# Kernel optimization log

Measured on AMD Instinct MI355X. Metric: run time of the kernel, lower is better.

Reference implementation:

```python
import jax, jax.numpy as jnp
import numpy as np

N_NODES = 50000
N_EDGES = 800000
IN, N1, N2, N3, N4, N5, L, NC = 7, 128, 128, 64, 64, 16, 16, 3


def _gat_params(key, fin, fout, edge_dim=1):
    ks = jax.random.split(key, 6)
    s = 0.1
    return dict(
        W=jax.random.normal(ks[0], (fin, fout), jnp.float32) * s,
        a_src=jax.random.normal(ks[1], (fout,), jnp.float32) * s,
        a_dst=jax.random.normal(ks[2], (fout,), jnp.float32) * s,
        We=jax.random.normal(ks[3], (edge_dim, fout), jnp.float32) * s,
        a_e=jax.random.normal(ks[4], (fout,), jnp.float32) * s,
        b=jax.random.normal(ks[5], (fout,), jnp.float32) * s,
    )


def setup_inputs() -> dict:
    key = jax.random.key(0)
    ks = jax.random.split(key, 16)
    inp = {
        'x1': jax.random.normal(ks[0], (N_NODES, IN), jnp.float32),
        'x2': jax.random.normal(ks[1], (N_NODES, IN), jnp.float32),
        'edge_index1': jax.random.randint(ks[2], (2, N_EDGES), 0, N_NODES),
        'edge_index2': jax.random.randint(ks[3], (2, N_EDGES), 0, N_NODES),
        'x_norm2_1': jax.random.normal(ks[4], (L,), jnp.float32),
        'x_norm2_2': jax.random.normal(ks[5], (L,), jnp.float32),
        'edge_col1': jax.random.uniform(ks[6], (N_EDGES, 1), jnp.float32),
        'edge_col2': jax.random.uniform(ks[7], (N_EDGES, 1), jnp.float32),
    }
    p1 = _gat_params(ks[8], IN, N1)
    p2 = _gat_params(ks[9], N1, N2)
    p3 = _gat_params(ks[10], N2, N3)
    for i, p in enumerate((p1, p2, p3), 1):
        for k, v in p.items():
            inp[f'{k}{i}'] = v
    s = 0.1
    inp['W_lin'] = jax.random.normal(ks[11], (N3 + L, N4), jnp.float32) * s
    inp['b_lin'] = jnp.zeros((N4,), jnp.float32)
    inp['W_c1'] = jax.random.normal(ks[12], (2 * N4, N5), jnp.float32) * s
    inp['b_c1'] = jnp.zeros((N5,), jnp.float32)
    inp['W_c2'] = jax.random.normal(ks[13], (N5, NC), jnp.float32) * s
    inp['b_c2'] = jnp.zeros((NC,), jnp.float32)
    return inp


def _gat_conv(x, src, dst, eattr, W, a_src, a_dst, We, a_e, b, n):
    # PyG GATConv, heads=1, add_self_loops with fill_value='mean'
    h = x @ W                                           # [N, C]
    ones = jnp.ones_like(dst, dtype=eattr.dtype)
    deg = jax.ops.segment_sum(ones, dst, n)
    loop_attr = jax.ops.segment_sum(eattr, dst, n) / jnp.maximum(deg, 1.0)[:, None]
    ar = jnp.arange(n, dtype=src.dtype)
    s = jnp.concatenate([src, ar])
    d = jnp.concatenate([dst, ar])
    ea = jnp.concatenate([eattr, loop_attr], axis=0)    # [E+N, edge_dim]
    alpha = (h @ a_src)[s] + (h @ a_dst)[d] + (ea @ We) @ a_e
    alpha = jax.nn.leaky_relu(alpha, 0.2)
    amax = jax.ops.segment_max(alpha, d, n)             # every node has a self loop
    ex = jnp.exp(alpha - amax[d])
    denom = jax.ops.segment_sum(ex, d, n)
    w = ex / denom[d]                                   # segment softmax weights
    out = jax.ops.segment_sum(w[:, None] * h[s], d, n)  # [N, C]
    return out + b


def _process_graph(x, ei, eattr, params):
    src, dst = ei[0], ei[1]
    n = x.shape[0]
    for p in params:
        x = jax.nn.elu(_gat_conv(x, src, dst, eattr, *p, n))
    return x.mean(axis=0)


def reference(x1, x2, edge_index1, edge_index2, x_norm2_1, x_norm2_2,
              edge_col1, edge_col2,
              W1, a_src1, a_dst1, We1, a_e1, b1,
              W2, a_src2, a_dst2, We2, a_e2, b2,
              W3, a_src3, a_dst3, We3, a_e3, b3,
              W_lin, b_lin, W_c1, b_c1, W_c2, b_c2):
    params = [
        (W1, a_src1, a_dst1, We1, a_e1, b1),
        (W2, a_src2, a_dst2, We2, a_e2, b2),
        (W3, a_src3, a_dst3, We3, a_e3, b3),
    ]
    g1 = _process_graph(x1, edge_index1, edge_col1, params)
    g2 = _process_graph(x2, edge_index2, edge_col2, params)
    g1 = jnp.concatenate([g1, x_norm2_1]) @ W_lin + b_lin
    g2 = jnp.concatenate([g2, x_norm2_2]) @ W_lin + b_lin
    x = jnp.concatenate([g1, g2])                       # [2*N4]
    h = jax.nn.relu(x @ W_c1 + b_c1)
    logits = h @ W_c2 + b_c2
    return logits[None, :]                              # [1, num_classes]
```

## Files before the change

kernel.cpp:

```cpp
#include <hip/hip_runtime.h>
#include <math.h>

#define NN 50000
#define NE 800000
#define NT 100000
#define NTP 100032
#define ET (2*NE + NT)
#define NPB 128
#define NBK 782
#define BCH 2048
#define BCAP 2816

typedef __attribute__((ext_vector_type(8))) short bf16x8;
typedef __attribute__((ext_vector_type(4))) float f32x4;

static __device__ __forceinline__ float wave_max64(float v){
  #pragma unroll
  for(int off=32;off;off>>=1) v = fmaxf(v, __shfl_xor(v,off));
  return v;
}
static __device__ __forceinline__ float wave_sum64(float v){
  #pragma unroll
  for(int off=32;off;off>>=1) v += __shfl_xor(v,off);
  return v;
}
static __device__ __forceinline__ unsigned short f2bf(float f){
  unsigned u = __float_as_uint(f);
  return (unsigned short)((u + 0x7FFFu + ((u>>16)&1u)) >> 16);
}
static __device__ __forceinline__ float bflo(unsigned v){ return __uint_as_float(v<<16); }
static __device__ __forceinline__ float bfhi(unsigned v){ return __uint_as_float(v & 0xFFFF0000u); }

__global__ __launch_bounds__(256) void k_hist(const int* __restrict__ d1,
    const int* __restrict__ d2, int* __restrict__ bcnt){
  __shared__ int h[1024];
  int t = threadIdx.x;
  #pragma unroll
  for (int i=0;i<4;i++) h[t + i*256] = 0;
  __syncthreads();
  int stride = gridDim.x*256;
  for (int e = blockIdx.x*256 + t; e < NE; e += stride){
    atomicAdd(&h[d1[e]>>7], 1);
    atomicAdd(&h[(d2[e]+NN)>>7], 1);
  }
  __syncthreads();
  #pragma unroll
  for (int i=0;i<4;i++){
    int idx = t + i*256;
    if (h[idx]) atomicAdd(&bcnt[idx], h[idx]);
  }
}

__global__ void k_hscan(const int* __restrict__ bcnt, int* __restrict__ hbase,
                        int* __restrict__ row_ptr){
  int t = threadIdx.x;
  int i0 = t*4;
  int c0=bcnt[i0], c1=bcnt[i0+1], c2=bcnt[i0+2], c3=bcnt[i0+3];
  int ts = c0+c1+c2+c3;
  int lane = t & 63, wv = t >> 6;
  int inc = ts;
  #pragma unroll
  for (int off=1; off<64; off<<=1){ int u = __shfl_up(inc, off); if (lane>=off) inc += u; }
  __shared__ int wsum[4];
  if (lane==63) wsum[wv] = inc;
  __syncthreads();
  int woff = 0;
  #pragma unroll
  for (int w=0; w<4; ++w) if (w < wv) woff += wsum[w];
  int run = woff + inc - ts;
  hbase[i0] = run; hbase[i0+1] = run+c0; hbase[i0+2] = run+c0+c1; hbase[i0+3] = run+c0+c1+c2;
  if (t==0) row_ptr[NT] = ET;
}

__global__ __launch_bounds__(256) void k_bin(const int* __restrict__ s1,
    const int* __restrict__ d1, const float* __restrict__ e1,
    const int* __restrict__ s2, const int* __restrict__ d2,
    const float* __restrict__ e2, const int* __restrict__ hbase,
    int* __restrict__ gcur, uint2* __restrict__ gstage){
  __shared__ int cnt[1024], loff[1024], cur[1024], gbase_sh[1024];
  __shared__ uint2 sdata[BCH];
  __shared__ unsigned short sbkt[BCH];
  __shared__ int wsum[4];
  int tid = threadIdx.x;
  int e0 = blockIdx.x*BCH;
  unsigned pack[8], eab[8];
  unsigned short bk[8];
  #pragma unroll
  for (int i=0;i<4;i++){ cnt[tid + i*256] = 0; cur[tid + i*256] = 0; }
  __syncthreads();
  #pragma unroll
  for (int u=0; u<8; ++u){
    int e = e0 + u*256 + tid;
    int b = NBK; unsigned p = 0, ea = 0;
    if (e < 2*NE){
      int src, dst; float eav;
      if (e < NE){ src = s1[e]; dst = d1[e]; eav = e1[e]; }
      else { int e2i = e - NE; src = s2[e2i] + NN; dst = d2[e2i] + NN; eav = e2[e2i]; }
      b = dst >> 7;
      p = (unsigned)src | ((unsigned)(dst & 127) << 17);
      ea = __float_as_uint(eav);
    }
    bk[u] = (unsigned short)b; pack[u] = p; eab[u] = ea;
    atomicAdd(&cnt[b], 1);
  }
  __syncthreads();
  {
    int i0 = tid*4;
    int c0=cnt[i0], c1=cnt[i0+1], c2=cnt[i0+2], c3=cnt[i0+3];
    int ts = c0+c1+c2+c3;
    int lane = tid & 63, wv = tid >> 6;
    int inc = ts;
    #pragma unroll
    for (int off=1; off<64; off<<=1){ int u = __shfl_up(inc, off); if (lane>=off) inc += u; }
    if (lane==63) wsum[wv] = inc;
    __syncthreads();
    int woff = 0;
    #pragma unroll
    for (int w=0; w<4; ++w) if (w < wv) woff += wsum[w];
    int run = woff + inc - ts;
    loff[i0] = run; loff[i0+1] = run+c0; loff[i0+2] = run+c0+c1; loff[i0+3] = run+c0+c1+c2;
  }
  for (int i = tid; i < NBK; i += 256)
    if (cnt[i] > 0) gbase_sh[i] = hbase[i] + atomicAdd(&gcur[i], cnt[i]);
  __syncthreads();
  #pragma unroll
  for (int u=0; u<8; ++u){
    int b = bk[u];
    int p = loff[b] + atomicAdd(&cur[b], 1);
    sdata[p] = make_uint2(pack[u], eab[u]);
    sbkt[p] = (unsigned short)b;
  }
  __syncthreads();
  for (int k = tid; k < BCH; k += 256){
    int b = sbkt[k];
    if (b < NBK) gstage[gbase_sh[b] + (k - loff[b])] = sdata[k];
  }
}

__global__ __launch_bounds__(256) void k_bucket(const uint2* __restrict__ gstage,
    const int* __restrict__ hbase, int2* __restrict__ srt, int* __restrict__ row_ptr){
  __shared__ uint2 sd[BCAP];
  __shared__ int deg[NPB], rbase[NPB], cur[NPB];
  __shared__ float easum[NPB];
  __shared__ int wsum[4];
  int b = blockIdx.x, t = threadIdx.x;
  int lo = b*NPB;
  int nloc = min(NPB, NT - lo);
  int est = hbase[b], ecnt = hbase[b+1] - est;
  bool inlds = (ecnt <= BCAP);
  if (t < NPB){ deg[t] = 0; easum[t] = 0.f; }
  __syncthreads();
  for (int k = t; k < ecnt; k += 256){
    uint2 v = gstage[est + k];
    if (inlds) sd[k] = v;
    int dl = v.x >> 17;
    atomicAdd(&deg[dl], 1);
    atomicAdd(&easum[dl], __uint_as_float(v.y));
  }
  __syncthreads();
  int dv = (t < nloc) ? deg[t] + 1 : 0;
  int lane = t & 63, wv = t >> 6;
  int inc = dv;
  #pragma unroll
  for (int off=1; off<64; off<<=1){ int u = __shfl_up(inc, off); if (lane>=off) inc += u; }
  if (lane==63) wsum[wv] = inc;
  __syncthreads();
  int woff = 0;
  #pragma unroll
  for (int w=0; w<4; ++w) if (w < wv) woff += wsum[w];
  int gb = est + lo + (woff + inc - dv);
  if (t < nloc){
    row_ptr[lo + t] = gb;
    rbase[t] = gb;
    cur[t] = 1;
    float se = easum[t] / fmaxf((float)deg[t], 1.f);
    srt[gb] = make_int2(lo + t, __float_as_int(se));
  }
  __syncthreads();
  for (int k = t; k < ecnt; k += 256){
    uint2 v = inlds ? sd[k] : gstage[est + k];
    int dl = v.x >> 17;
    int pos = rbase[dl] + atomicAdd(&cur[dl], 1);
    srt[pos] = make_int2((int)(v.x & 0x1FFFFu), (int)v.y);
  }
}

__global__ __launch_bounds__(256) void k_prep(
    const float* __restrict__ We0, const float* __restrict__ ae0,
    const float* __restrict__ We1, const float* __restrict__ ae1,
    const float* __restrict__ We2, const float* __restrict__ ae2,
    float* __restrict__ ce3, int* __restrict__ zbase,
    const float* __restrict__ W1, const float* __restrict__ W2,
    unsigned short* __restrict__ Wt1, unsigned short* __restrict__ Wt2){
  int t = threadIdx.x;
  for (int i = t; i < 1024+1024+128; i += 256) zbase[i] = 0;
  if (t < 64){
    const float* We[3] = {We0, We1, We2};
    const float* ae[3] = {ae0, ae1, ae2};
    const int fo[3] = {128, 128, 64};
    for (int L = 0; L < 3; ++L){
      float s = 0.f;
      for (int c = t; c < fo[L]; c += 64) s += We[L][c]*ae[L][c];
      s = wave_sum64(s);
      if (t == 0) ce3[L] = s;
    }
  }
  for (int i = t; i < 128*128; i += 256){
    int c = i >> 7, k = i & 127;
    Wt1[c*136 + k] = f2bf(W1[k*128 + c]);
  }
  for (int i = t; i < 64*128; i += 256){
    int c = i >> 7, k = i & 127;
    Wt2[c*136 + k] = f2bf(W2[k*64 + c]);
  }
}

template<int N>
__global__ __launch_bounds__(256) void k_gemm_mfma(
    const unsigned short* __restrict__ x16, const unsigned short* __restrict__ Wt,
    const float* __restrict__ a_src, const float* __restrict__ a_dst,
    unsigned short* __restrict__ h16, float* __restrict__ hs,
    float* __restrict__ hd, int n){
  constexpr int CT = N/16;
  __shared__ unsigned short Wl[N*136];
  int tid = threadIdx.x;
  for (int i = tid; i < N*136/8; i += 256)
    ((uint4*)Wl)[i] = ((const uint4*)Wt)[i];
  __syncthreads();
  int lane = tid & 63, w = tid >> 6;
  int arow = blockIdx.x*64 + w*16 + (lane & 15);
  int kb   = (lane >> 4) * 8;
  int rsafe = (arow < n) ? arow : (n-1);
  f32x4 acc[CT] = {};
  #pragma unroll
  for (int s = 0; s < 4; ++s){
    bf16x8 a = *(const bf16x8*)(x16 + (size_t)rsafe*128 + s*32 + kb);
    #pragma unroll
    for (int c = 0; c < CT; ++c){
      bf16x8 b = *(const bf16x8*)(&Wl[(c*16 + (lane&15))*136 + s*32 + kb]);
      acc[c] = __builtin_amdgcn_mfma_f32_16x16x32_bf16(a, b, acc[c], 0, 0, 0);
    }
  }
  int drow = blockIdx.x*64 + w*16 + (lane>>4)*4;
  int dcol = lane & 15;
  float psv[4] = {0,0,0,0}, pdv[4] = {0,0,0,0};
  #pragma unroll
  for (int c = 0; c < CT; ++c){
    float as = a_src[c*16 + dcol], ad = a_dst[c*16 + dcol];
    #pragma unroll
    for (int j = 0; j < 4; ++j){
      float v = acc[c][j];
      if (drow + j < n) h16[(size_t)(drow+j)*N + c*16 + dcol] = f2bf(v);
      psv[j] += v*as; pdv[j] += v*ad;
    }
  }
  #pragma unroll
  for (int off = 1; off < 16; off <<= 1){
    #pragma unroll
    for (int j=0;j<4;j++){ psv[j] += __shfl_xor(psv[j], off); pdv[j] += __shfl_xor(pdv[j], off); }
  }
  if (dcol == 0){
    #pragma unroll
    for (int j=0;j<4;j++) if (drow+j < n){ hs[drow+j] = psv[j]; hd[drow+j] = pdv[j]; }
  }
}

__global__ __launch_bounds__(256) void k_gemm7(const float* __restrict__ x1,
    const float* __restrict__ x2, const float* __restrict__ W,
    const float* __restrict__ a_src, const float* __restrict__ a_dst,
    unsigned short* __restrict__ h16, float* __restrict__ hs,
    float* __restrict__ hd, int n){
  __shared__ float Wl[7][128];
  int tid = threadIdx.x;
  for (int i = tid; i < 7*128; i += 256) ((float*)Wl)[i] = W[i];
  __syncthreads();
  int tx = tid & 31, ty = tid >> 5;
  int r = blockIdx.x*8 + ty;
  if (r >= n) return;
  const float* xr = (r < NN) ? (x1 + (size_t)r*7) : (x2 + (size_t)(r-NN)*7);
  float xv[7];
  #pragma unroll
  for (int k=0;k<7;k++) xv[k] = xr[k];
  float4 s = make_float4(0.f,0.f,0.f,0.f);
  #pragma unroll
  for (int k=0;k<7;k++){
    float4 wv = *(const float4*)(&Wl[k][tx*4]);
    s.x += xv[k]*wv.x; s.y += xv[k]*wv.y; s.z += xv[k]*wv.z; s.w += xv[k]*wv.w;
  }
  unsigned r0p = (unsigned)f2bf(s.x) | ((unsigned)f2bf(s.y)<<16);
  unsigned r1p = (unsigned)f2bf(s.z) | ((unsigned)f2bf(s.w)<<16);
  *(uint2*)(h16 + (size_t)r*128 + tx*4) = make_uint2(r0p, r1p);
  float ps = s.x*a_src[tx*4] + s.y*a_src[tx*4+1] + s.z*a_src[tx*4+2] + s.w*a_src[tx*4+3];
  float pd = s.x*a_dst[tx*4] + s.y*a_dst[tx*4+1] + s.z*a_dst[tx*4+2] + s.w*a_dst[tx*4+3];
  #pragma unroll
  for (int off=16; off; off>>=1){ ps += __shfl_xor(ps, off); pd += __shfl_xor(pd, off); }
  if (tx==0){ hs[r] = ps; hd[r] = pd; }
}

template<int FOUT, bool OBF>
__global__ __launch_bounds__(256) void k_aggregate(const unsigned short* __restrict__ h16,
    const float* __restrict__ hs, const float* __restrict__ hd,
    const int2* __restrict__ srt, const int* __restrict__ row_ptr,
    const float* __restrict__ ce_p, const float* __restrict__ b,
    void* __restrict__ xout, int n){
  constexpr int LPE = FOUT/8;
  constexpr int EPS = 64/LPE;
  __shared__ float s_p[4][64];
  __shared__ int   s_s[4][64];
  int tid = threadIdx.x;
  int wv = tid >> 6, lane = tid & 63;
  int wid = (int)((blockIdx.x*256 + tid) >> 6);
  if (wid >= n) return;
  float ce  = *ce_p;
  int beg = row_ptr[wid], end = row_ptr[wid+1];
  float hdn = hd[wid];
  int e_sub = lane / LPE;
  int col8  = (lane % LPE) * 8;
  float m = -INFINITY, den = 0.f;
  float acc[8] = {0.f,0.f,0.f,0.f,0.f,0.f,0.f,0.f};
  for (int base = beg; base < end; base += 64){
    int slot = base + lane;
    float a = -INFINITY; int src = 0;
    if (slot < end){
      int2 pk = srt[slot];
      src = pk.x;
      a = hs[src] + hdn + __int_as_float(pk.y)*ce;
      a = (a > 0.f) ? a : 0.2f*a;
    }
    float cm = wave_max64(a);
    float mnew = fmaxf(m, cm);
    float scale = __expf(m - mnew);
    den *= scale;
    #pragma unroll
    for (int u=0;u<8;u++) acc[u] *= scale;
    float p = __expf(a - mnew);
    den += wave_sum64(p);
    s_p[wv][lane] = p; s_s[wv][lane] = src;
    asm volatile("s_waitcnt lgkmcnt(0)" ::: "memory");
    int cnt = end - base; if (cnt > 64) cnt = 64;
    for (int j = 0; j < cnt; j += 2*EPS){
      int jj0 = j + e_sub, jj1 = j + EPS + e_sub;
      float p0 = s_p[wv][jj0];  int sj0 = s_s[wv][jj0];
      float p1 = s_p[wv][jj1];  int sj1 = s_s[wv][jj1];
      uint4 h0 = *(const uint4*)(h16 + (size_t)sj0*FOUT + col8);
      uint4 h1 = *(const uint4*)(h16 + (size_t)sj1*FOUT + col8);
      acc[0] += p0*bflo(h0.x); acc[1] += p0*bfhi(h0.x);
      acc[2] += p0*bflo(h0.y); acc[3] += p0*bfhi(h0.y);
      acc[4] += p0*bflo(h0.z); acc[5] += p0*bfhi(h0.z);
      acc[6] += p0*bflo(h0.w); acc[7] += p0*bfhi(h0.w);
      acc[0] += p1*bflo(h1.x); acc[1] += p1*bfhi(h1.x);
      acc[2] += p1*bflo(h1.y); acc[3] += p1*bfhi(h1.y);
      acc[4] += p1*bflo(h1.z); acc[5] += p1*bfhi(h1.z);
      acc[6] += p1*bflo(h1.w); acc[7] += p1*bfhi(h1.w);
    }
    m = mnew;
  }
  #pragma unroll
  for (int off = LPE; off < 64; off <<= 1){
    #pragma unroll
    for (int u=0;u<8;u++) acc[u] += __shfl_xor(acc[u], off);
  }
  float inv = 1.f/den;
  if (lane < LPE){
    float o[8];
    #pragma unroll
    for (int u=0;u<8;u++){
      o[u] = acc[u]*inv + b[col8+u];
      o[u] = (o[u] > 0.f) ? o[u] : (__expf(o[u]) - 1.f);
    }
    if (OBF){
      uint4 pkd;
      pkd.x = (unsigned)f2bf(o[0]) | ((unsigned)f2bf(o[1])<<16);
      pkd.y = (unsigned)f2bf(o[2]) | ((unsigned)f2bf(o[3])<<16);
      pkd.z = (unsigned)f2bf(o[4]) | ((unsigned)f2bf(o[5])<<16);
      pkd.w = (unsigned)f2bf(o[6]) | ((unsigned)f2bf(o[7])<<16);
      *(uint4*)((unsigned short*)xout + (size_t)wid*FOUT + col8) = pkd;
    } else {
      float4 o0 = make_float4(o[0],o[1],o[2],o[3]);
      float4 o1 = make_float4(o[4],o[5],o[6],o[7]);
      *(float4*)((float*)xout + (size_t)wid*FOUT + col8)     = o0;
      *(float4*)((float*)xout + (size_t)wid*FOUT + col8 + 4) = o1;
    }
  }
}

__global__ __launch_bounds__(256) void k_colsum2(const float* __restrict__ x,
    float* __restrict__ gsum, int n){
  __shared__ float ls[128];
  int t = threadIdx.x;
  if (t < 128) ls[t] = 0.f;
  __syncthreads();
  int c4 = (t & 15) * 4;
  int rsub = t >> 4;
  float4 s1 = make_float4(0.f,0.f,0.f,0.f), s2 = make_float4(0.f,0.f,0.f,0.f);
  for (int r = blockIdx.x*16 + rsub; r < n; r += gridDim.x*16){
    float4 v = *(const float4*)(x + (size_t)r*64 + c4);
    if (r < NN){ s1.x+=v.x; s1.y+=v.y; s1.z+=v.z; s1.w+=v.w; }
    else       { s2.x+=v.x; s2.y+=v.y; s2.z+=v.z; s2.w+=v.w; }
  }
  atomicAdd(&ls[c4+0], s1.x); atomicAdd(&ls[c4+1], s1.y);
  atomicAdd(&ls[c4+2], s1.z); atomicAdd(&ls[c4+3], s1.w);
  atomicAdd(&ls[64+c4+0], s2.x); atomicAdd(&ls[64+c4+1], s2.y);
  atomicAdd(&ls[64+c4+2], s2.z); atomicAdd(&ls[64+c4+3], s2.w);
  __syncthreads();
  if (t < 128) atomicAdd(&gsum[t], ls[t]);
}

__global__ void k_head(const float* __restrict__ gs1, const float* __restrict__ gs2,
                       const float* __restrict__ xn1, const float* __restrict__ xn2,
                       const float* __restrict__ Wlin, const float* __restrict__ blin,
                       const float* __restrict__ Wc1, const float* __restrict__ bc1,
                       const float* __restrict__ Wc2, const float* __restrict__ bc2,
                       float* __restrict__ out){
  __shared__ float c1[80], c2[80], xcat[128], hb[16];
  int tid = threadIdx.x;
  const float invn = 1.f/(float)NN;
  if (tid < 64){ c1[tid] = gs1[tid]*invn; c2[tid] = gs2[tid]*invn; }
  else if (tid < 80){ c1[tid] = xn1[tid-64]; c2[tid] = xn2[tid-64]; }
  __syncthreads();
  if (tid < 64){
    float s = blin[tid];
    for (int k=0;k<80;k++) s += c1[k]*Wlin[k*64+tid];
    xcat[tid] = s;
  } else {
    int j = tid - 64;
    float s = blin[j];
    for (int k=0;k<80;k++) s += c2[k]*Wlin[k*64+j];
    xcat[tid] = s;
  }
  __syncthreads();
  if (tid < 16){
    float s = bc1[tid];
    for (int k=0;k<128;k++) s += xcat[k]*Wc1[k*16+tid];
    hb[tid] = fmaxf(s, 0.f);
  }
  __syncthreads();
  if (tid < 3){
    float s = bc2[tid];
    for (int k=0;k<16;k++) s += hb[k]*Wc2[k*3+tid];
    out[tid] = s;
  }
}

extern "C" void kernel_launch(void* const* d_in, const int* in_sizes, int n_in,
                              void* d_out, int out_size, void* d_ws, size_t ws_size,
                              hipStream_t stream){
  const float* x1  = (const float*)d_in[0];
  const float* x2  = (const float*)d_in[1];
  const int*   ei1 = (const int*)d_in[2];
  const int*   ei2 = (const int*)d_in[3];
  const float* xn1 = (const float*)d_in[4];
  const float* xn2 = (const float*)d_in[5];
  const float* ec1 = (const float*)d_in[6];
  const float* ec2 = (const float*)d_in[7];
  const float* W[3]    = {(const float*)d_in[8],  (const float*)d_in[14], (const float*)d_in[20]};
  const float* asrc[3] = {(const float*)d_in[9],  (const float*)d_in[15], (const float*)d_in[21]};
  const float* adst[3] = {(const float*)d_in[10], (const float*)d_in[16], (const float*)d_in[22]};
  const float* We[3]   = {(const float*)d_in[11], (const float*)d_in[17], (const float*)d_in[23]};
  const float* ae[3]   = {(const float*)d_in[12], (const float*)d_in[18], (const float*)d_in[24]};
  const float* bb[3]   = {(const float*)d_in[13], (const float*)d_in[19], (const float*)d_in[25]};
  const float* Wlin = (const float*)d_in[26];
  const float* blin = (const float*)d_in[27];
  const float* Wc1  = (const float*)d_in[28];
  const float* bc1  = (const float*)d_in[29];
  const float* Wc2  = (const float*)d_in[30];
  const float* bc2  = (const float*)d_in[31];
  float* out = (float*)d_out;

  char* wsb = (char*)d_ws;
  unsigned short* x16   = (unsigned short*)wsb;
  uint2*          gstage = (uint2*)wsb;
  float*          bufX  = (float*)wsb;
  unsigned short* h16  = (unsigned short*)(wsb + (size_t)NTP*128*2);
  int2*           srt  = (int2*)(wsb + (size_t)NTP*128*2 + (size_t)NT*128*2);
  float* hs   = (float*)(srt + ET);
  float* hd   = hs + NT;
  int*   row_ptr = (int*)(hd + NT);
  int*   bcnt  = row_ptr + NT + 2;
  int*   gcur  = bcnt + 1024;
  float* gsum  = (float*)(gcur + 1024);
  int*   hbase = (int*)(gsum + 128);
  float* ce3   = (float*)(hbase + 1024);
  unsigned short* Wt1 = (unsigned short*)(ce3 + 8);
  unsigned short* Wt2 = Wt1 + 128*136;

  const int* s1 = ei1, * d1 = ei1 + NE;
  const int* s2 = ei2, * d2 = ei2 + NE;

  k_prep<<<1, 256, 0, stream>>>(We[0], ae[0], We[1], ae[1], We[2], ae[2], ce3,
                                bcnt, W[1], W[2], Wt1, Wt2);

  k_hist<<<256, 256, 0, stream>>>(d1, d2, bcnt);
  k_hscan<<<1, 256, 0, stream>>>(bcnt, hbase, row_ptr);
  k_bin<<<(2*NE + BCH - 1)/BCH, 256, 0, stream>>>(s1, d1, ec1, s2, d2, ec2, hbase, gcur, gstage);
  k_bucket<<<NBK, 256, 0, stream>>>(gstage, hbase, srt, row_ptr);

  k_gemm7<<<(NT+7)/8, 256, 0, stream>>>(x1, x2, W[0], asrc[0], adst[0], h16, hs, hd, NT);
  k_aggregate<128,true><<<(NT+3)/4, 256, 0, stream>>>(h16, hs, hd, srt, row_ptr, ce3+0, bb[0], x16, NT);
  k_gemm_mfma<128><<<(NT+63)/64, 256, 0, stream>>>(x16, Wt1, asrc[1], adst[1], h16, hs, hd, NT);
  k_aggregate<128,true><<<(NT+3)/4, 256, 0, stream>>>(h16, hs, hd, srt, row_ptr, ce3+1, bb[1], x16, NT);
  k_gemm_mfma<64><<<(NT+63)/64, 256, 0, stream>>>(x16, Wt2, asrc[2], adst[2], h16, hs, hd, NT);
  k_aggregate<64,false><<<(NT+3)/4, 256, 0, stream>>>(h16, hs, hd, srt, row_ptr, ce3+2, bb[2], bufX, NT);

  k_colsum2<<<512, 256, 0, stream>>>(bufX, gsum, NT);
  k_head<<<1, 128, 0, stream>>>(gsum, gsum+64, xn1, xn2, Wlin, blin, Wc1, bc1, Wc2, bc2, out);
}
```

Baseline: 457.5 us.

## Process four row tiles per wave in MFMA GEMM and guard odd-edge loads

The MFMA GEMM kernel now computes four 16-row tiles per wave (256 rows per block), so each B fragment read from shared memory is reused across four MFMAs and the per-block weight staging is amortized over more rows. This cuts the grid size by four and raises accumulator register use, which may lower occupancy. Separately, the aggregation inner loop now skips the second gathered row load when it would fall past the segment end. Before, that load fetched an invalid slot and relied on a zero weight to cancel it.

```diff
diff --git a/kernel.cpp b/kernel.cpp
--- a/kernel.cpp
+++ b/kernel.cpp
@@ -228,40 +228,51 @@
     ((uint4*)Wl)[i] = ((const uint4*)Wt)[i];
   __syncthreads();
   int lane = tid & 63, w = tid >> 6;
-  int arow = blockIdx.x*64 + w*16 + (lane & 15);
   int kb   = (lane >> 4) * 8;
-  int rsafe = (arow < n) ? arow : (n-1);
-  f32x4 acc[CT] = {};
+  int l15  = lane & 15;
+  int rbase0 = blockIdx.x*256 + w*16;
+  f32x4 acc[4][CT] = {};
   #pragma unroll
   for (int s = 0; s < 4; ++s){
-    bf16x8 a = *(const bf16x8*)(x16 + (size_t)rsafe*128 + s*32 + kb);
+    bf16x8 a[4];
+    #pragma unroll
+    for (int rt = 0; rt < 4; ++rt){
+      int arow = rbase0 + rt*64 + l15;
+      int rsafe = (arow < n) ? arow : (n-1);
+      a[rt] = *(const bf16x8*)(x16 + (size_t)rsafe*128 + s*32 + kb);
+    }
     #pragma unroll
     for (int c = 0; c < CT; ++c){
-      bf16x8 b = *(const bf16x8*)(&Wl[(c*16 + (lane&15))*136 + s*32 + kb]);
-      acc[c] = __builtin_amdgcn_mfma_f32_16x16x32_bf16(a, b, acc[c], 0, 0, 0);
-    }
-  }
-  int drow = blockIdx.x*64 + w*16 + (lane>>4)*4;
+      bf16x8 b = *(const bf16x8*)(&Wl[(c*16 + l15)*136 + s*32 + kb]);
+      #pragma unroll
+      for (int rt = 0; rt < 4; ++rt)
+        acc[rt][c] = __builtin_amdgcn_mfma_f32_16x16x32_bf16(a[rt], b, acc[rt][c], 0, 0, 0);
+    }
+  }
   int dcol = lane & 15;
-  float psv[4] = {0,0,0,0}, pdv[4] = {0,0,0,0};
-  #pragma unroll
-  for (int c = 0; c < CT; ++c){
-    float as = a_src[c*16 + dcol], ad = a_dst[c*16 + dcol];
-    #pragma unroll
-    for (int j = 0; j < 4; ++j){
-      float v = acc[c][j];
-      if (drow + j < n) h16[(size_t)(drow+j)*N + c*16 + dcol] = f2bf(v);
-      psv[j] += v*as; pdv[j] += v*ad;
-    }
-  }
-  #pragma unroll
-  for (int off = 1; off < 16; off <<= 1){
-    #pragma unroll
-    for (int j=0;j<4;j++){ psv[j] += __shfl_xor(psv[j], off); pdv[j] += __shfl_xor(pdv[j], off); }
-  }
-  if (dcol == 0){
-    #pragma unroll
-    for (int j=0;j<4;j++) if (drow+j < n){ hs[drow+j] = psv[j]; hd[drow+j] = pdv[j]; }
+  #pragma unroll
+  for (int rt = 0; rt < 4; ++rt){
+    int drow = rbase0 + rt*64 + (lane>>4)*4;
+    float psv[4] = {0,0,0,0}, pdv[4] = {0,0,0,0};
+    #pragma unroll
+    for (int c = 0; c < CT; ++c){
+      float as = a_src[c*16 + dcol], ad = a_dst[c*16 + dcol];
+      #pragma unroll
+      for (int j = 0; j < 4; ++j){
+        float v = acc[rt][c][j];
+        if (drow + j < n) h16[(size_t)(drow+j)*N + c*16 + dcol] = f2bf(v);
+        psv[j] += v*as; pdv[j] += v*ad;
+      }
+    }
+    #pragma unroll
+    for (int off = 1; off < 16; off <<= 1){
+      #pragma unroll
+      for (int j=0;j<4;j++){ psv[j] += __shfl_xor(psv[j], off); pdv[j] += __shfl_xor(pdv[j], off); }
+    }
+    if (dcol == 0){
+      #pragma unroll
+      for (int j=0;j<4;j++) if (drow+j < n){ hs[drow+j] = psv[j]; hd[drow+j] = pdv[j]; }
+    }
   }
 }
 
@@ -339,19 +350,27 @@
     asm volatile("s_waitcnt lgkmcnt(0)" ::: "memory");
     int cnt = end - base; if (cnt > 64) cnt = 64;
     for (int j = 0; j < cnt; j += 2*EPS){
-      int jj0 = j + e_sub, jj1 = j + EPS + e_sub;
+      int jj0 = j + e_sub;
       float p0 = s_p[wv][jj0];  int sj0 = s_s[wv][jj0];
-      float p1 = s_p[wv][jj1];  int sj1 = s_s[wv][jj1];
       uint4 h0 = *(const uint4*)(h16 + (size_t)sj0*FOUT + col8);
-      uint4 h1 = *(const uint4*)(h16 + (size_t)sj1*FOUT + col8);
-      acc[0] += p0*bflo(h0.x); acc[1] += p0*bfhi(h0.x);
-      acc[2] += p0*bflo(h0.y); acc[3] += p0*bfhi(h0.y);
-      acc[4] += p0*bflo(h0.z); acc[5] += p0*bfhi(h0.z);
-      acc[6] += p0*bflo(h0.w); acc[7] += p0*bfhi(h0.w);
-      acc[0] += p1*bflo(h1.x); acc[1] += p1*bfhi(h1.x);
-      acc[2] += p1*bflo(h1.y); acc[3] += p1*bfhi(h1.y);
-      acc[4] += p1*bflo(h1.z); acc[5] += p1*bfhi(h1.z);
-      acc[6] += p1*bflo(h1.w); acc[7] += p1*bfhi(h1.w);
+      if (j + EPS < cnt){
+        int jj1 = j + EPS + e_sub;
+        float p1 = s_p[wv][jj1];  int sj1 = s_s[wv][jj1];
+        uint4 h1 = *(const uint4*)(h16 + (size_t)sj1*FOUT + col8);
+        acc[0] += p0*bflo(h0.x); acc[1] += p0*bfhi(h0.x);
+        acc[2] += p0*bflo(h0.y); acc[3] += p0*bfhi(h0.y);
+        acc[4] += p0*bflo(h0.z); acc[5] += p0*bfhi(h0.z);
+        acc[6] += p0*bflo(h0.w); acc[7] += p0*bfhi(h0.w);
+        acc[0] += p1*bflo(h1.x); acc[1] += p1*bfhi(h1.x);
+        acc[2] += p1*bflo(h1.y); acc[3] += p1*bfhi(h1.y);
+        acc[4] += p1*bflo(h1.z); acc[5] += p1*bfhi(h1.z);
+        acc[6] += p1*bflo(h1.w); acc[7] += p1*bfhi(h1.w);
+      } else {
+        acc[0] += p0*bflo(h0.x); acc[1] += p0*bfhi(h0.x);
+        acc[2] += p0*bflo(h0.y); acc[3] += p0*bfhi(h0.y);
+        acc[4] += p0*bflo(h0.z); acc[5] += p0*bfhi(h0.z);
+        acc[6] += p0*bflo(h0.w); acc[7] += p0*bfhi(h0.w);
+      }
     }
     m = mnew;
   }
@@ -497,9 +516,9 @@
 
   k_gemm7<<<(NT+7)/8, 256, 0, stream>>>(x1, x2, W[0], asrc[0], adst[0], h16, hs, hd, NT);
   k_aggregate<128,true><<<(NT+3)/4, 256, 0, stream>>>(h16, hs, hd, srt, row_ptr, ce3+0, bb[0], x16, NT);
-  k_gemm_mfma<128><<<(NT+63)/64, 256, 0, stream>>>(x16, Wt1, asrc[1], adst[1], h16, hs, hd, NT);
+  k_gemm_mfma<128><<<(NT+255)/256, 256, 0, stream>>>(x16, Wt1, asrc[1], adst[1], h16, hs, hd, NT);
   k_aggregate<128,true><<<(NT+3)/4, 256, 0, stream>>>(h16, hs, hd, srt, row_ptr, ce3+1, bb[1], x16, NT);
-  k_gemm_mfma<64><<<(NT+63)/64, 256, 0, stream>>>(x16, Wt2, asrc[2], adst[2], h16, hs, hd, NT);
+  k_gemm_mfma<64><<<(NT+255)/256, 256, 0, stream>>>(x16, Wt2, asrc[2], adst[2], h16, hs, hd, NT);
   k_aggregate<64,false><<<(NT+3)/4, 256, 0, stream>>>(h16, hs, hd, srt, row_ptr, ce3+2, bb[2], bufX, NT);
 
   k_colsum2<<<512, 256, 0, stream>>>(bufX, gsum, NT);
```

Measured after the change: 485.5 us. 6.1% more time.
